# Optimization experiments

Measured on AMD Instinct MI355X. Metric: run time of the kernel, lower is better.

Reference implementation:

```python
import jax, jax.numpy as jnp
import numpy as np

K = 31      # avg_pool2d kernel
PAD = 15    # padding; PyTorch avg_pool2d default count_include_pad=True -> divide by K*K always


def _avg_pool_31(t):
    # windowed sum with zero padding, then fixed divisor K*K (count_include_pad=True)
    s = jax.lax.reduce_window(
        t, 0.0, jax.lax.add,
        window_dimensions=(1, 1, K, K),
        window_strides=(1, 1, 1, 1),
        padding=[(0, 0), (0, 0), (PAD, PAD), (PAD, PAD)],
    )
    return s / (K * K)


def setup_inputs() -> dict:
    key = jax.random.key(0)
    k1, k2 = jax.random.split(key)
    logits = jax.random.normal(k1, (32, 1, 512, 512), dtype=jnp.float32)
    targets = jax.random.uniform(k2, (32, 1, 512, 512), dtype=jnp.float32)
    return {"logits": logits, "targets": targets}


def reference(logits, targets):
    B = targets.shape[0]
    weight = 1.0 + 5.0 * jnp.abs(_avg_pool_31(targets) - targets)
    # numerically stable BCE-with-logits, reduction='none'
    bce = jnp.maximum(logits, 0.0) - logits * targets + jnp.log1p(jnp.exp(-jnp.abs(logits)))
    w = weight.reshape(B, -1)
    num = (w * bce.reshape(B, -1)).sum(axis=1)
    den = w.sum(axis=1)
    return (num / den).sum() / B
```

## Files before the change

### kernel.cpp

```cpp
#include <hip/hip_runtime.h>
#include <math.h>

#define BATCH 32
#define H 512
#define W 512
#define PAD 15
#define BAND 8
#define NBANDS (H / BAND)
#define NBLOCKS (BATCH * NBANDS)
#define NTHREADS 512
#define NPART (NBLOCKS * 8)
#define NXCD 8
#define INV_KK (1.0f / 961.0f)

#define EMIT(tv, lv, hs)                                                      \
    {                                                                         \
        float pooled_ = (hs) * INV_KK;                                        \
        float wgt_ = fmaf(5.f, fabsf(pooled_ - (tv)), 1.f);                   \
        float al_ = fabsf(lv);                                                \
        float bce_ = fmaxf((lv), 0.f) - (lv) * (tv)                           \
                     + __logf(1.f + __expf(-al_));                            \
        num = fmaf(wgt_, bce_, num);                                          \
        den += wgt_;                                                          \
    }

#define KSLOT(pk, pkm1, tv, lv, FIRST, LAST)                                  \
    {                                                                         \
        float hs_ = base_;                                                    \
        if (!(LAST)) {                                                        \
            float sa_ = __shfl_up(tot_ - (pk), 2);                            \
            hs_ += okm2 ? sa_ : 0.f;                                          \
        }                                                                     \
        if (!(FIRST)) {                                                       \
            float se_ = __shfl_down((pkm1), 2);                               \
            hs_ += okp2 ? se_ : 0.f;                                          \
        }                                                                     \
        EMIT(tv, lv, hs_)                                                     \
    }

#define ROWPASS(r)                                                            \
    {                                                                         \
        const float4* lp_ = (const float4*)(lb + (size_t)(y0 + (r)) * W + x0);\
        float4 La_ = lp_[0], Lb_ = lp_[1];                                    \
        float4 A_  = ((const float4*)vs[(r)])[2 * lane];                      \
        float4 B_  = ((const float4*)vs[(r)])[2 * lane + 1];                  \
        float4 Ta_ = ((const float4*)traw[(r)])[2 * lane];                    \
        float4 Tb_ = ((const float4*)traw[(r)])[2 * lane + 1];                \
        const float p0_ = A_.x;                                               \
        const float p1_ = p0_ + A_.y;                                         \
        const float p2_ = p1_ + A_.z;                                         \
        const float p3_ = p2_ + A_.w;                                         \
        const float p4_ = p3_ + B_.x;                                         \
        const float p5_ = p4_ + B_.y;                                         \
        const float p6_ = p5_ + B_.z;                                         \
        const float tot_ = p6_ + B_.w;                                        \
        const float bm_ = __shfl_up(tot_, 1);                                 \
        const float dp_ = __shfl_down(tot_, 1);                               \
        const float base_ = (okm1 ? bm_ : 0.f) + tot_ + (okp1 ? dp_ : 0.f);   \
        KSLOT(p0_, 0.f, Ta_.x, La_.x, 1, 0)                                   \
        KSLOT(p1_, p0_, Ta_.y, La_.y, 0, 0)                                   \
        KSLOT(p2_, p1_, Ta_.z, La_.z, 0, 0)                                   \
        KSLOT(p3_, p2_, Ta_.w, La_.w, 0, 0)                                   \
        KSLOT(p4_, p3_, Tb_.x, Lb_.x, 0, 0)                                   \
        KSLOT(p5_, p4_, Tb_.y, Lb_.y, 0, 0)                                   \
        KSLOT(p6_, p5_, Tb_.z, Lb_.z, 0, 0)                                   \
        KSLOT(0.f, p6_, Tb_.w, Lb_.w, 0, 1)                                   \
    }

#define P1_INIT(G, C0, C1)                                                    \
    _Pragma("unroll")                                                         \
    for (int c = (C0); c < (C1); ++c) {                                       \
        const int y = y0 + c - PAD;                                           \
        float a0 = 0.f;                                                       \
        if ((G) || (unsigned)y < (unsigned)H) a0 = tcol[y * W];               \
        run0 += a0;                                                           \
        if (c >= PAD && c < PAD + BAND) traw[c - PAD][tid] = a0;              \
    }

#define P1_SLIDE(G, J0, J1)                                                   \
    _Pragma("unroll")                                                         \
    for (int j = (J0); j < (J1); ++j) {                                       \
        vs[j][tid] = run0;                                                    \
        if (j < BAND - 1) {                                                   \
            const int ye = y0 + j + PAD + 1, yl = y0 + j - PAD;               \
            float e0 = 0.f, s0 = 0.f;                                         \
            if ((G) || (unsigned)ye < (unsigned)H) e0 = tcol[ye * W];         \
            if ((G) || (unsigned)yl < (unsigned)H) s0 = tcol[yl * W];         \
            run0 += e0 - s0;                                                  \
        }                                                                     \
    }

#define PHASE1(G)                                                             \
    P1_INIT(G, 0, 8)   __builtin_amdgcn_sched_barrier(0);                     \
    P1_INIT(G, 8, 16)  __builtin_amdgcn_sched_barrier(0);                     \
    P1_INIT(G, 16, 24) __builtin_amdgcn_sched_barrier(0);                     \
    P1_INIT(G, 24, 31) __builtin_amdgcn_sched_barrier(0);                     \
    P1_SLIDE(G, 0, 4)  __builtin_amdgcn_sched_barrier(0);                     \
    P1_SLIDE(G, 4, 8)

__global__ __launch_bounds__(NTHREADS)
void wbce_band_kernel(const float* __restrict__ logits,
                      const float* __restrict__ targets,
                      float2* __restrict__ partials) {
    __shared__ __align__(16) float vs[BAND][W];
    __shared__ __align__(16) float traw[BAND][W];

    const int tid  = threadIdx.x;
    const int lane = tid & 63;
    const int w    = tid >> 6;

    const int bid  = (int)blockIdx.x;
    const int sbid = (bid & (NXCD - 1)) * (NBLOCKS / NXCD) + (bid >> 3);

    const int img  = sbid >> 6;
    const int band = sbid & (NBANDS - 1);
    const int y0   = band * BAND;
    const int x0   = lane * 8;

    const float* tb = targets + (size_t)img * H * W;
    const float* lb = logits  + (size_t)img * H * W;
    const float* tcol = tb + tid;

    float run0 = 0.f;
    if (y0 >= PAD && y0 + BAND + PAD - 1 < H) {
        PHASE1(1)
    } else {
        PHASE1(0)
    }
    __syncthreads();

    const bool okm2 = lane >= 2, okm1 = lane >= 1;
    const bool okp1 = lane <= 62, okp2 = lane <= 61;
    float num = 0.f, den = 0.f;

    ROWPASS(w)

    #pragma unroll
    for (int off = 32; off > 0; off >>= 1) {
        num += __shfl_down(num, off);
        den += __shfl_down(den, off);
    }
    if (lane == 0) {
        partials[sbid * 8 + w] = make_float2(num, den);
    }
}

__global__ __launch_bounds__(1024)
void wbce_finalize_kernel(const float2* __restrict__ partials,
                          float* __restrict__ out) {
    __shared__ float rsum[16];
    const int t = threadIdx.x;
    const int img = t >> 5;
    const int j = t & 31;
    const int base = img * 512;
    float num = 0.f, den = 0.f;
    #pragma unroll
    for (int k = 0; k < 16; ++k) {
        float2 p = partials[base + j + 32 * k];
        num += p.x; den += p.y;
    }
    #pragma unroll
    for (int off = 16; off > 0; off >>= 1) {
        num += __shfl_down(num, off, 32);
        den += __shfl_down(den, off, 32);
    }
    float ratio = 0.f;
    if ((t & 31) == 0) ratio = num / den;
    ratio += __shfl_down(ratio, 32);
    const int lane = t & 63;
    const int wv = t >> 6;
    if (lane == 0) rsum[wv] = ratio;
    __syncthreads();
    if (t == 0) {
        float s = 0.f;
        #pragma unroll
        for (int i = 0; i < 16; ++i) s += rsum[i];
        out[0] = s / (float)BATCH;
    }
}

extern "C" void kernel_launch(void* const* d_in, const int* in_sizes, int n_in,
                              void* d_out, int out_size, void* d_ws, size_t ws_size,
                              hipStream_t stream) {
    const float* logits  = (const float*)d_in[0];
    const float* targets = (const float*)d_in[1];
    float* out = (float*)d_out;
    float2* partials = (float2*)d_ws;

    wbce_band_kernel<<<NBLOCKS, NTHREADS, 0, stream>>>(logits, targets, partials);
    wbce_finalize_kernel<<<1, 1024, 0, stream>>>(partials, out);
}
```

Measured before the change: 23.72 us.

## Prefetch logits before pooling phase and pre-reduce partials per block

```diff
diff --git a/kernel.cpp b/kernel.cpp
--- a/kernel.cpp
+++ b/kernel.cpp
@@ -9,7 +9,6 @@
 #define NBANDS (H / BAND)
 #define NBLOCKS (BATCH * NBANDS)
 #define NTHREADS 512
-#define NPART (NBLOCKS * 8)
 #define NXCD 8
 #define INV_KK (1.0f / 961.0f)
 
@@ -38,10 +37,8 @@
         EMIT(tv, lv, hs_)                                                     \
     }
 
-#define ROWPASS(r)                                                            \
+#define ROWPASS(r, La_, Lb_)                                                  \
     {                                                                         \
-        const float4* lp_ = (const float4*)(lb + (size_t)(y0 + (r)) * W + x0);\
-        float4 La_ = lp_[0], Lb_ = lp_[1];                                    \
         float4 A_  = ((const float4*)vs[(r)])[2 * lane];                      \
         float4 B_  = ((const float4*)vs[(r)])[2 * lane + 1];                  \
         float4 Ta_ = ((const float4*)traw[(r)])[2 * lane];                    \
@@ -104,6 +101,7 @@
                       float2* __restrict__ partials) {
     __shared__ __align__(16) float vs[BAND][W];
     __shared__ __align__(16) float traw[BAND][W];
+    __shared__ float2 rnd[8];
 
     const int tid  = threadIdx.x;
     const int lane = tid & 63;
@@ -121,6 +119,10 @@
     const float* lb = logits  + (size_t)img * H * W;
     const float* tcol = tb + tid;
 
+    const float4* lp_ = (const float4*)(lb + (size_t)(y0 + w) * W + x0);
+    float4 Lpa = lp_[0], Lpb = lp_[1];
+    __builtin_amdgcn_sched_barrier(0);
+
     float run0 = 0.f;
     if (y0 >= PAD && y0 + BAND + PAD - 1 < H) {
         PHASE1(1)
@@ -133,15 +135,20 @@
     const bool okp1 = lane <= 62, okp2 = lane <= 61;
     float num = 0.f, den = 0.f;
 
-    ROWPASS(w)
+    ROWPASS(w, Lpa, Lpb)
 
     #pragma unroll
     for (int off = 32; off > 0; off >>= 1) {
         num += __shfl_down(num, off);
         den += __shfl_down(den, off);
     }
-    if (lane == 0) {
-        partials[sbid * 8 + w] = make_float2(num, den);
+    if (lane == 0) rnd[w] = make_float2(num, den);
+    __syncthreads();
+    if (tid == 0) {
+        float n = 0.f, d = 0.f;
+        #pragma unroll
+        for (int i = 0; i < 8; ++i) { n += rnd[i].x; d += rnd[i].y; }
+        partials[sbid] = make_float2(n, d);
     }
 }
 
@@ -150,15 +157,10 @@
                           float* __restrict__ out) {
     __shared__ float rsum[16];
     const int t = threadIdx.x;
-    const int img = t >> 5;
-    const int j = t & 31;
-    const int base = img * 512;
-    float num = 0.f, den = 0.f;
-    #pragma unroll
-    for (int k = 0; k < 16; ++k) {
-        float2 p = partials[base + j + 32 * k];
-        num += p.x; den += p.y;
-    }
+    float2 pa = partials[t * 2];
+    float2 pb = partials[t * 2 + 1];
+    float num = pa.x + pb.x;
+    float den = pa.y + pb.y;
     #pragma unroll
     for (int off = 16; off > 0; off >>= 1) {
         num += __shfl_down(num, off, 32);
```

Result: slower. 25.24 us (+6.4%).
